# Kernel optimization log

Hardware: AMD Instinct MI355X
Metric: run time of the kernel (lower is better)

## Reference

```python
import jax, jax.numpy as jnp
import numpy as np

N, E, D, H, O, G = 50000, 800000, 64, 64, 32, 64


def setup_inputs() -> dict:
    key = jax.random.key(0)
    ks = jax.random.split(key, 12)
    x = jax.random.normal(ks[0], (N, D), dtype=jnp.float32)
    edge_index = jax.random.randint(ks[1], (2, E), 0, N)
    batch = jnp.sort(jax.random.randint(ks[2], (N,), 0, G))

    def glorot(k, fan_in, fan_out):
        s = np.sqrt(6.0 / (fan_in + fan_out)).astype(np.float32)
        return jax.random.uniform(k, (fan_in, fan_out), jnp.float32, -s, s)

    return {
        "x": x,
        "edge_index": edge_index,
        "batch": batch,
        "W1": glorot(ks[3], D, H), "b1": jnp.zeros((H,), jnp.float32),
        "W2": glorot(ks[4], H, H), "b2": jnp.zeros((H,), jnp.float32),
        "W3": glorot(ks[5], H, H), "b3": jnp.zeros((H,), jnp.float32),
        "Wl": glorot(ks[6], H, O), "bl": jnp.zeros((O,), jnp.float32),
    }


def reference(x, edge_index, batch, W1, b1, W2, b2, W3, b3, Wl, bl):
    n = x.shape[0]
    # GCNConv default: add self-loops, symmetric deg^-1/2 normalization
    loop = jnp.arange(n, dtype=edge_index.dtype)
    src = jnp.concatenate([edge_index[0], loop])  # [E+N]
    dst = jnp.concatenate([edge_index[1], loop])
    deg = jax.ops.segment_sum(jnp.ones_like(src, dtype=x.dtype), dst, num_segments=n)
    dis = jax.lax.rsqrt(deg)  # deg >= 1 due to self-loops
    norm = (dis[src] * dis[dst])[:, None]  # [E+N, 1]

    def gcn(h, W, b):
        hw = h @ W                      # [N, H] small GEMM
        msg = hw[src] * norm            # gather + scale: [E+N, H]
        agg = jax.ops.segment_sum(msg, dst, num_segments=n)  # scatter-add
        return agg + b

    h = jax.nn.relu(gcn(x, W1, b1))
    h = jax.nn.relu(gcn(h, W2, b2))
    h = gcn(h, W3, b3)

    # global_mean_pool over graph ids
    counts = jax.ops.segment_sum(jnp.ones((n,), h.dtype), batch, num_segments=G)
    pooled = jax.ops.segment_sum(h, batch, num_segments=G) / counts[:, None]

    # dropout(p=0.5) is identity in eval mode
    return pooled @ Wl + bl
```

## Files before the change

kernel.cpp:

```cpp
#include <hip/hip_runtime.h>

#define HD 64
#define PSUB 16
#define NBLK 256
#define LOG_NBLK 8
#define NBKT 512

__device__ __forceinline__ unsigned short f2bf(float f) {
    union { float f; unsigned u; } v; v.f = f;
    unsigned r = v.u + 0x7FFF + ((v.u >> 16) & 1);
    return (unsigned short)(r >> 16);
}
__device__ __forceinline__ float u2f(unsigned u) {
    union { unsigned u; float f; } v; v.u = u;
    return v.f;
}


__global__ __launch_bounds__(256) void hist1_k(const int* __restrict__ dst,
                                               int* __restrict__ hist, int E, int chunk,
                                               float* __restrict__ partial, int psz)
{
    __shared__ int lh[NBKT];
    int t = threadIdx.x;
    for (int i = t; i < NBKT; i += 256) lh[i] = 0;
    for (int i = blockIdx.x * 256 + t; i < psz; i += gridDim.x * 256)
        partial[i] = 0.f;
    __syncthreads();
    int base = blockIdx.x * chunk;
    int end  = min(base + chunk, E);
    for (int i = base + t; i < end; i += 256)
        atomicAdd(&lh[dst[i] >> 7], 1);
    __syncthreads();
    for (int i = t; i < NBKT; i += 256)
        hist[blockIdx.x * NBKT + i] = lh[i];
}

__global__ __launch_bounds__(256) void scanA_k(const int* __restrict__ hist,
                                               int* __restrict__ tsum)
{
    __shared__ int s[256];
    int t = threadIdx.x;
    int l = blockIdx.x * 256 + t;
    int phys = (l & (NBLK - 1)) * NBKT + (l >> LOG_NBLK);
    s[t] = hist[phys];
    __syncthreads();
    for (int off = 128; off > 0; off >>= 1) {
        if (t < off) s[t] += s[t + off];
        __syncthreads();
    }
    if (t == 0) tsum[blockIdx.x] = s[0];
}

__global__ __launch_bounds__(1024) void scanB_k(int* __restrict__ tsum, int nb,
    const int* __restrict__ batch, int* __restrict__ gstart, int n, int G)
{
    __shared__ int s[1024];
    int t = threadIdx.x;
    int v = (t < nb) ? tsum[t] : 0;
    s[t] = v;
    __syncthreads();
    for (int off = 1; off < 1024; off <<= 1) {
        int u = (t >= off) ? s[t - off] : 0;
        __syncthreads();
        s[t] += u;
        __syncthreads();
    }
    if (t < nb) tsum[t] = s[t] - v;
    if (t <= G) {
        if (t == G) gstart[t] = n;
        else {
            int lo = 0, hi = n;
            while (lo < hi) { int m = (lo + hi) >> 1; if (batch[m] < t) lo = m + 1; else hi = m; }
            gstart[t] = lo;
        }
    }
}

__global__ __launch_bounds__(256) void scanC_k(const int* __restrict__ hist,
                                               const int* __restrict__ tsum,
                                               int* __restrict__ scanned)
{
    __shared__ int s[256];
    int t = threadIdx.x;
    int l = blockIdx.x * 256 + t;
    int phys = (l & (NBLK - 1)) * NBKT + (l >> LOG_NBLK);
    int own = hist[phys];
    s[t] = own;
    __syncthreads();
    for (int off = 1; off < 256; off <<= 1) {
        int u = (t >= off) ? s[t - off] : 0;
        __syncthreads();
        s[t] += u;
        __syncthreads();
    }
    scanned[l] = tsum[blockIdx.x] + s[t] - own;
}

__global__ __launch_bounds__(256) void append_k(const int* __restrict__ src,
    const int* __restrict__ dst, const int* __restrict__ scanned,
    int* __restrict__ pairs, int E, int chunk)
{
    __shared__ int cur[NBKT];
    int t = threadIdx.x;
    int blk = blockIdx.x;
    for (int i = t; i < NBKT; i += 256) cur[i] = scanned[i * NBLK + blk];
    __syncthreads();
    int base = blk * chunk;
    int end  = min(base + chunk, E);
    for (int i = base + t; i < end; i += 256) {
        int s = src[i], d = dst[i];
        int p = atomicAdd(&cur[d >> 7], 1);
        pairs[p] = (s << 7) | (d & 127);
    }
}

__global__ __launch_bounds__(256) void bucket_csr_k(const int* __restrict__ pairs,
    const int* __restrict__ scanned, int* __restrict__ offsets,
    float* __restrict__ dis, int* __restrict__ csr_src, int N, int E)
{
    __shared__ int cnt[128];
    __shared__ int sc[128];
    __shared__ int cur[128];
    int t = threadIdx.x;
    int b = blockIdx.x;
    int nodeBase = b * 128;
    int nNodes = min(128, N - nodeBase);
    int bBase = scanned[b * NBLK];
    int bEnd  = (b + 1 < NBKT) ? scanned[(b + 1) * NBLK] : E;

    if (t < 128) cnt[t] = 0;
    __syncthreads();
    for (int i = bBase + t; i < bEnd; i += 256)
        atomicAdd(&cnt[pairs[i] & 127], 1);
    __syncthreads();
    int myc = (t < 128) ? cnt[t] : 0;
    if (t < 128) sc[t] = myc;
    __syncthreads();
    for (int off = 1; off < 128; off <<= 1) {
        int u = (t < 128 && t >= off) ? sc[t - off] : 0;
        __syncthreads();
        if (t < 128) sc[t] += u;
        __syncthreads();
    }
    if (t < 128) {
        int excl = sc[t] - myc;
        cur[t] = excl;
        if (t < nNodes) {
            offsets[nodeBase + t] = bBase + excl;
            dis[nodeBase + t] = rsqrtf(1.0f + (float)myc);
        }
    }
    if (t == 0 && b == gridDim.x - 1) offsets[N] = E;
    __syncthreads();
    for (int i = bBase + t; i < bEnd; i += 256) {
        int pk = pairs[i];
        int pos = bBase + atomicAdd(&cur[pk & 127], 1);
        csr_src[pos] = ((unsigned)pk) >> 7;
    }
}


__global__ __launch_bounds__(256) void gemm64_k(
    const float* __restrict__ in, const float* __restrict__ W,
    const float* __restrict__ dis, unsigned short* __restrict__ outb, int n)
{
    __shared__ float HsT[HD][68];
    __shared__ float Ws[HD][HD];
    int t = threadIdx.x;
    int rowBase = blockIdx.x * 64;

    for (int i = t; i < HD * HD / 4; i += 256)
        ((float4*)Ws)[i] = ((const float4*)W)[i];

    if (blockIdx.x == 0 && t < 64)
        outb[(size_t)n * HD + t] = 0;

    {
        int k0 = (t & 15) * 4;
        for (int it = 0; it < 4; ++it) {
            int r = (t >> 4) + it * 16;
            int row = rowBase + r;
            float4 v = make_float4(0.f, 0.f, 0.f, 0.f);
            if (row < n)
                v = *(const float4*)&in[(size_t)row * HD + k0];
            HsT[k0 + 0][r] = v.x;
            HsT[k0 + 1][r] = v.y;
            HsT[k0 + 2][r] = v.z;
            HsT[k0 + 3][r] = v.w;
        }
    }
    __syncthreads();

    int c4 = (t & 15) * 4;
    int r4 = (t >> 4) * 4;
    float acc[4][4];
    #pragma unroll
    for (int i = 0; i < 4; ++i)
        #pragma unroll
        for (int j = 0; j < 4; ++j) acc[i][j] = 0.f;

    #pragma unroll 8
    for (int k = 0; k < HD; ++k) {
        float4 a = *(const float4*)&HsT[k][r4];
        float4 b = *(const float4*)&Ws[k][c4];
        acc[0][0] += a.x * b.x; acc[0][1] += a.x * b.y; acc[0][2] += a.x * b.z; acc[0][3] += a.x * b.w;
        acc[1][0] += a.y * b.x; acc[1][1] += a.y * b.y; acc[1][2] += a.y * b.z; acc[1][3] += a.y * b.w;
        acc[2][0] += a.z * b.x; acc[2][1] += a.z * b.y; acc[2][2] += a.z * b.z; acc[2][3] += a.z * b.w;
        acc[3][0] += a.w * b.x; acc[3][1] += a.w * b.y; acc[3][2] += a.w * b.z; acc[3][3] += a.w * b.w;
    }

    #pragma unroll
    for (int i = 0; i < 4; ++i) {
        int row = rowBase + r4 + i;
        if (row < n) {
            float ds = dis[row];
            ushort4 o;
            o.x = f2bf(ds * acc[i][0]); o.y = f2bf(ds * acc[i][1]);
            o.z = f2bf(ds * acc[i][2]); o.w = f2bf(ds * acc[i][3]);
            *(ushort4*)&outb[(size_t)row * HD + c4] = o;
        }
    }
}

__device__ __forceinline__ void gather8(const unsigned short* __restrict__ hwb,
    const int* __restrict__ offsets, const int* __restrict__ csr_src,
    int node, bool act, int n, int fl, float* a )
{
    int beg = 0, end = 0;
    if (act) { beg = offsets[node]; end = offsets[node + 1]; }
    int deg = end - beg;
    int md = deg;
    md = max(md, __shfl_xor(md, 8, 64));
    md = max(md, __shfl_xor(md, 16, 64));
    md = max(md, __shfl_xor(md, 32, 64));

    int nodeC = act ? node : n;
    uint4 sv = *(const uint4*)(hwb + ((size_t)nodeC << 6) + (fl << 3));
    a[0] = u2f(sv.x << 16); a[1] = u2f(sv.x & 0xFFFF0000u);
    a[2] = u2f(sv.y << 16); a[3] = u2f(sv.y & 0xFFFF0000u);
    a[4] = u2f(sv.z << 16); a[5] = u2f(sv.z & 0xFFFF0000u);
    a[6] = u2f(sv.w << 16); a[7] = u2f(sv.w & 0xFFFF0000u);

    int grpbase = threadIdx.x & 56;
    int idxv = (fl < deg) ? csr_src[beg + fl] : n;
    for (int jb = 0; jb < md; jb += 8) {
        int e2 = jb + 8 + fl;
        int nidx = (e2 < deg) ? csr_src[beg + e2] : n;
        uint4 g[8];
        #pragma unroll
        for (int j = 0; j < 8; ++j) {
            int row = __shfl(idxv, grpbase + j, 64);
            g[j] = *(const uint4*)(hwb + ((size_t)row << 6) + (fl << 3));
        }
        #pragma unroll
        for (int j = 0; j < 8; ++j) {
            a[0] += u2f(g[j].x << 16); a[1] += u2f(g[j].x & 0xFFFF0000u);
            a[2] += u2f(g[j].y << 16); a[3] += u2f(g[j].y & 0xFFFF0000u);
            a[4] += u2f(g[j].z << 16); a[5] += u2f(g[j].z & 0xFFFF0000u);
            a[6] += u2f(g[j].w << 16); a[7] += u2f(g[j].w & 0xFFFF0000u);
        }
        idxv = nidx;
    }
}

__global__ __launch_bounds__(256) void agg_gemm_k(
    const unsigned short* __restrict__ hwb, const float* __restrict__ dis,
    const int* __restrict__ offsets, const int* __restrict__ csr_src,
    const float* __restrict__ b_prev, const float* __restrict__ W,
    unsigned short* __restrict__ outb, int n)
{
    __shared__ float As[32][68];
    __shared__ float Ws[HD][HD];
    int t    = threadIdx.x;
    int lane = t & 63;
    int grp  = lane >> 3;
    int fl   = lane & 7;
    int w    = t >> 6;
    int nib  = w * 8 + grp;
    int nodeBase = blockIdx.x * 32;
    int node = nodeBase + nib;
    bool act = node < n;

    for (int i = t; i < HD * HD / 4; i += 256)
        ((float4*)Ws)[i] = ((const float4*)W)[i];

    if (blockIdx.x == 0 && t < 64)
        outb[(size_t)n * HD + t] = 0;

    float a[8];
    gather8(hwb, offsets, csr_src, node, act, n, fl, a);

    float ds = act ? dis[node] : 0.f;
    int c0 = fl << 3;
    float4 b0 = *(const float4*)&b_prev[c0];
    float4 b1 = *(const float4*)&b_prev[c0 + 4];
    float4 v0, v1;
    v0.x = fmaxf(a[0] * ds + b0.x, 0.f); v0.y = fmaxf(a[1] * ds + b0.y, 0.f);
    v0.z = fmaxf(a[2] * ds + b0.z, 0.f); v0.w = fmaxf(a[3] * ds + b0.w, 0.f);
    v1.x = fmaxf(a[4] * ds + b1.x, 0.f); v1.y = fmaxf(a[5] * ds + b1.y, 0.f);
    v1.z = fmaxf(a[6] * ds + b1.z, 0.f); v1.w = fmaxf(a[7] * ds + b1.w, 0.f);
    *(float4*)&As[nib][c0]     = v0;
    *(float4*)&As[nib][c0 + 4] = v1;
    __syncthreads();

    int r  = t & 31;
    int c8 = (t >> 5) << 3;
    float s0 = 0.f, s1 = 0.f, s2 = 0.f, s3 = 0.f, s4 = 0.f, s5 = 0.f, s6 = 0.f, s7 = 0.f;
    #pragma unroll 4
    for (int k = 0; k < HD; k += 4) {
        float4 aa = *(const float4*)&As[r][k];
        #pragma unroll
        for (int kk = 0; kk < 4; ++kk) {
            float av = (kk == 0) ? aa.x : (kk == 1) ? aa.y : (kk == 2) ? aa.z : aa.w;
            float4 w0 = *(const float4*)&Ws[k + kk][c8];
            float4 w1 = *(const float4*)&Ws[k + kk][c8 + 4];
            s0 += av * w0.x; s1 += av * w0.y; s2 += av * w0.z; s3 += av * w0.w;
            s4 += av * w1.x; s5 += av * w1.y; s6 += av * w1.z; s7 += av * w1.w;
        }
    }
    int orow = nodeBase + r;
    if (orow < n) {
        float d2 = dis[orow];
        ushort4 o0, o1;
        o0.x = f2bf(d2 * s0); o0.y = f2bf(d2 * s1); o0.z = f2bf(d2 * s2); o0.w = f2bf(d2 * s3);
        o1.x = f2bf(d2 * s4); o1.y = f2bf(d2 * s5); o1.z = f2bf(d2 * s6); o1.w = f2bf(d2 * s7);
        *(ushort4*)&outb[(size_t)orow * HD + c8]     = o0;
        *(ushort4*)&outb[(size_t)orow * HD + c8 + 4] = o1;
    }
}

__global__ __launch_bounds__(256) void agg_pool8_k(const unsigned short* __restrict__ hwb,
    const float* __restrict__ dis, const int* __restrict__ offsets,
    const int* __restrict__ csr_src, const int* __restrict__ batch,
    float* __restrict__ partial, int n)
{
    __shared__ float sh[32][68];
    __shared__ int gids[32];
    __shared__ int allsame;
    int t    = threadIdx.x;
    int lane = t & 63;
    int grp  = lane >> 3;
    int fl   = lane & 7;
    int w    = t >> 6;
    int nib  = w * 8 + grp;
    int node = blockIdx.x * 32 + nib;
    bool act = node < n;

    float a[8];
    gather8(hwb, offsets, csr_src, node, act, n, fl, a);

    float ds = act ? dis[node] : 0.f;
    int c0 = fl << 3;
    *(float4*)&sh[nib][c0]     = make_float4(a[0] * ds, a[1] * ds, a[2] * ds, a[3] * ds);
    *(float4*)&sh[nib][c0 + 4] = make_float4(a[4] * ds, a[5] * ds, a[6] * ds, a[7] * ds);
    if (fl == 0) gids[nib] = act ? batch[node] : -1;
    __syncthreads();

    if (t == 0) {
        int g0 = gids[0];
        int ok = (g0 >= 0);
        #pragma unroll
        for (int r = 1; r < 32; ++r) ok &= (gids[r] == g0);
        allsame = ok;
    }
    __syncthreads();

    int slot = blockIdx.x & (PSUB - 1);
    if (allsame) {
        if (t < 64) {
            float s = 0.f;
            #pragma unroll
            for (int r = 0; r < 32; ++r) s += sh[r][t];
            atomicAdd(&partial[((size_t)gids[0] * PSUB + slot) * HD + t], s);
        }
    } else {
        int c  = lane;
        int r0 = w * 8;
        int gw = gids[r0];
        bool same8 = (gw >= 0);
        #pragma unroll
        for (int rr = 1; rr < 8; ++rr) same8 &= (gids[r0 + rr] == gw);
        if (same8) {
            float v = 0.f;
            #pragma unroll
            for (int rr = 0; rr < 8; ++rr) v += sh[r0 + rr][c];
            atomicAdd(&partial[((size_t)gw * PSUB + slot) * HD + c], v);
        } else {
            #pragma unroll
            for (int rr = 0; rr < 8; ++rr) {
                int gg = gids[r0 + rr];
                if (gg >= 0)
                    atomicAdd(&partial[((size_t)gg * PSUB + slot) * HD + c], sh[r0 + rr][c]);
            }
        }
    }
}

__global__ __launch_bounds__(64) void pool2_k(const float* __restrict__ partial,
    const int* __restrict__ gstart, const float* __restrict__ b3,
    const float* __restrict__ Wl, const float* __restrict__ bl,
    float* __restrict__ out, int O)
{
    __shared__ float pooled[HD];
    int g = blockIdx.x;
    int t = threadIdx.x;
    float sum = 0.0f;
    #pragma unroll
    for (int s = 0; s < PSUB; ++s)
        sum += partial[((size_t)g * PSUB + s) * HD + t];
    float cnt = (float)(gstart[g + 1] - gstart[g]);
    pooled[t] = sum / cnt + b3[t];
    __syncthreads();
    if (t < O) {
        float acc = bl[t];
        #pragma unroll
        for (int k = 0; k < HD; ++k) acc += pooled[k] * Wl[k * O + t];
        out[g * O + t] = acc;
    }
}

extern "C" void kernel_launch(void* const* d_in, const int* in_sizes, int n_in,
                              void* d_out, int out_size, void* d_ws, size_t ws_size,
                              hipStream_t stream)
{
    const float* x    = (const float*)d_in[0];
    const int*   ei   = (const int*)d_in[1];
    const int*   batch= (const int*)d_in[2];
    const float* W1   = (const float*)d_in[3];
    const float* b1   = (const float*)d_in[4];
    const float* W2   = (const float*)d_in[5];
    const float* b2   = (const float*)d_in[6];
    const float* W3   = (const float*)d_in[7];
    const float* b3   = (const float*)d_in[8];
    const float* Wl   = (const float*)d_in[9];
    const float* bl   = (const float*)d_in[10];
    float* out = (float*)d_out;

    const int N = in_sizes[0] / HD;
    const int E = in_sizes[1] / 2;
    const int O = in_sizes[10];
    const int G = out_size / O;

    const int* src = ei;
    const int* dst = ei + E;

    char* p = (char*)d_ws;
    auto take = [&](size_t bytes) { char* r = p; p += (bytes + 255) & ~(size_t)255; return r; };
    int*   csr_src = (int*)  take((size_t)(E + 256) * 4);
    int*   offsets = (int*)  take((size_t)(N + 1) * 4);
    float* dis     = (float*)take((size_t)N * 4);
    int*   gstart  = (int*)  take((size_t)(G + 1) * 4);
    float* partial = (float*)take((size_t)G * PSUB * HD * 4);
    unsigned short* hwb  = (unsigned short*)take((size_t)(N + 1) * HD * 2);
    unsigned short* hwb2 = (unsigned short*)take((size_t)(N + 1) * HD * 2);

    int* pairs   = (int*)hwb;
    int* hist    = (int*)hwb2;
    int* scanned = hist + NBLK * NBKT;
    int* tsum    = scanned + NBLK * NBKT;

    const int TB = 256;
    int chunk   = (E + NBLK - 1) / NBLK;
    int ntiles  = (NBLK * NBKT) / 256;
    int nb_gemm = (N + 63) / 64;
    int nb_agg8 = (N + 31) / 32;
    int nbuck   = (N + 127) / 128;
    int psz     = G * PSUB * HD;

    hist1_k<<<NBLK, TB, 0, stream>>>(dst, hist, E, chunk, partial, psz);
    scanA_k<<<ntiles, TB, 0, stream>>>(hist, tsum);
    scanB_k<<<1, 1024, 0, stream>>>(tsum, ntiles, batch, gstart, N, G);
    scanC_k<<<ntiles, TB, 0, stream>>>(hist, tsum, scanned);
    append_k<<<NBLK, TB, 0, stream>>>(src, dst, scanned, pairs, E, chunk);
    bucket_csr_k<<<nbuck, TB, 0, stream>>>(pairs, scanned, offsets, dis, csr_src, N, E);

    gemm64_k<<<nb_gemm, TB, 0, stream>>>(x, W1, dis, hwb, N);

    agg_gemm_k<<<nb_agg8, TB, 0, stream>>>(hwb, dis, offsets, csr_src, b1, W2, hwb2, N);

    agg_gemm_k<<<nb_agg8, TB, 0, stream>>>(hwb2, dis, offsets, csr_src, b2, W3, hwb, N);

    agg_pool8_k<<<nb_agg8, TB, 0, stream>>>(hwb, dis, offsets, csr_src, batch, partial, N);

    pool2_k<<<G, 64, 0, stream>>>(partial, gstart, b3, Wl, bl, out, O);
}
```

Baseline: 184.9 us.

## Reorder nodes by graph and degree bins to balance gather warps

Builds a permutation of nodes, sorted by (graph id, clamped in-degree), using a histogram, a scan and a scatter pass. The aggregation kernels then process nodes in this order, so the 8 nodes sharing a wavefront have similar degree and less time is lost waiting on the longest neighbour list. Nodes stay grouped by graph, which keeps the pooling fast path usable. The cost is two extra kernel launches, atomics during CSR build, an indirect node lookup, and scattered output writes that no longer hit consecutive rows.

```diff
diff --git a/kernel.cpp b/kernel.cpp
--- a/kernel.cpp
+++ b/kernel.cpp
@@ -5,6 +5,7 @@
 #define NBLK 256
 #define LOG_NBLK 8
 #define NBKT 512
+#define DBINS 64
 
 __device__ __forceinline__ unsigned short f2bf(float f) {
     union { float f; unsigned u; } v; v.f = f;
@@ -19,13 +20,16 @@
 
 __global__ __launch_bounds__(256) void hist1_k(const int* __restrict__ dst,
                                                int* __restrict__ hist, int E, int chunk,
-                                               float* __restrict__ partial, int psz)
+                                               float* __restrict__ partial, int psz,
+                                               int* __restrict__ bins, int nbins2)
 {
     __shared__ int lh[NBKT];
     int t = threadIdx.x;
     for (int i = t; i < NBKT; i += 256) lh[i] = 0;
     for (int i = blockIdx.x * 256 + t; i < psz; i += gridDim.x * 256)
         partial[i] = 0.f;
+    for (int i = blockIdx.x * 256 + t; i < nbins2; i += gridDim.x * 256)
+        bins[i] = 0;
     __syncthreads();
     int base = blockIdx.x * chunk;
     int end  = min(base + chunk, E);
@@ -117,7 +121,8 @@
 
 __global__ __launch_bounds__(256) void bucket_csr_k(const int* __restrict__ pairs,
     const int* __restrict__ scanned, int* __restrict__ offsets,
-    float* __restrict__ dis, int* __restrict__ csr_src, int N, int E)
+    float* __restrict__ dis, int* __restrict__ csr_src,
+    const int* __restrict__ batch, int* __restrict__ bins, int N, int E)
 {
     __shared__ int cnt[128];
     __shared__ int sc[128];
@@ -147,8 +152,10 @@
         int excl = sc[t] - myc;
         cur[t] = excl;
         if (t < nNodes) {
-            offsets[nodeBase + t] = bBase + excl;
-            dis[nodeBase + t] = rsqrtf(1.0f + (float)myc);
+            int node = nodeBase + t;
+            offsets[node] = bBase + excl;
+            dis[node] = rsqrtf(1.0f + (float)myc);
+            atomicAdd(&bins[batch[node] * DBINS + min(myc, DBINS - 1)], 1);
         }
     }
     if (t == 0 && b == gridDim.x - 1) offsets[N] = E;
@@ -158,6 +165,47 @@
         int pos = bBase + atomicAdd(&cur[pk & 127], 1);
         csr_src[pos] = ((unsigned)pk) >> 7;
     }
+}
+
+__global__ __launch_bounds__(1024) void binscan_k(int* __restrict__ bins, int nbins)
+{
+    __shared__ int s[1024];
+    int t = threadIdx.x;
+    int per = (nbins + 1023) >> 10;
+    int b0 = t * per;
+    int v[8];
+    int sum = 0;
+    for (int i = 0; i < per; ++i) {
+        int idx = b0 + i;
+        v[i] = (idx < nbins) ? bins[idx] : 0;
+        sum += v[i];
+    }
+    s[t] = sum;
+    __syncthreads();
+    for (int off = 1; off < 1024; off <<= 1) {
+        int u = (t >= off) ? s[t - off] : 0;
+        __syncthreads();
+        s[t] += u;
+        __syncthreads();
+    }
+    int run = s[t] - sum;
+    for (int i = 0; i < per; ++i) {
+        int idx = b0 + i;
+        if (idx < nbins) bins[idx] = run;
+        run += v[i];
+    }
+}
+
+__global__ __launch_bounds__(256) void permscat_k(const int* __restrict__ offsets,
+    const int* __restrict__ batch, const int* __restrict__ binbase,
+    int* __restrict__ bincur, int* __restrict__ perm, int N)
+{
+    int i = blockIdx.x * 256 + threadIdx.x;
+    if (i >= N) return;
+    int deg = offsets[i + 1] - offsets[i];
+    int bin = batch[i] * DBINS + min(deg, DBINS - 1);
+    int pos = binbase[bin] + atomicAdd(&bincur[bin], 1);
+    perm[pos] = i;
 }
 
 
@@ -234,7 +282,6 @@
     md = max(md, __shfl_xor(md, 8, 64));
     md = max(md, __shfl_xor(md, 16, 64));
     md = max(md, __shfl_xor(md, 32, 64));
-
     int nodeC = act ? node : n;
     uint4 sv = *(const uint4*)(hwb + ((size_t)nodeC << 6) + (fl << 3));
     a[0] = u2f(sv.x << 16); a[1] = u2f(sv.x & 0xFFFF0000u);
@@ -267,11 +314,13 @@
 __global__ __launch_bounds__(256) void agg_gemm_k(
     const unsigned short* __restrict__ hwb, const float* __restrict__ dis,
     const int* __restrict__ offsets, const int* __restrict__ csr_src,
+    const int* __restrict__ perm,
     const float* __restrict__ b_prev, const float* __restrict__ W,
     unsigned short* __restrict__ outb, int n)
 {
     __shared__ float As[32][68];
     __shared__ float Ws[HD][HD];
+    __shared__ int pnode[32];
     int t    = threadIdx.x;
     int lane = t & 63;
     int grp  = lane >> 3;
@@ -279,15 +328,18 @@
     int w    = t >> 6;
     int nib  = w * 8 + grp;
     int nodeBase = blockIdx.x * 32;
-    int node = nodeBase + nib;
-    bool act = node < n;
+    bool act = (nodeBase + nib) < n;
+
+    if (t < 32) pnode[t] = (nodeBase + t < n) ? perm[nodeBase + t] : 0;
 
     for (int i = t; i < HD * HD / 4; i += 256)
         ((float4*)Ws)[i] = ((const float4*)W)[i];
 
     if (blockIdx.x == 0 && t < 64)
         outb[(size_t)n * HD + t] = 0;
-
+    __syncthreads();
+
+    int node = pnode[nib];
     float a[8];
     gather8(hwb, offsets, csr_src, node, act, n, fl, a);
 
@@ -319,8 +371,8 @@
             s4 += av * w1.x; s5 += av * w1.y; s6 += av * w1.z; s7 += av * w1.w;
         }
     }
-    int orow = nodeBase + r;
-    if (orow < n) {
+    if (nodeBase + r < n) {
+        int orow = pnode[r];
         float d2 = dis[orow];
         ushort4 o0, o1;
         o0.x = f2bf(d2 * s0); o0.y = f2bf(d2 * s1); o0.z = f2bf(d2 * s2); o0.w = f2bf(d2 * s3);
@@ -332,11 +384,12 @@
 
 __global__ __launch_bounds__(256) void agg_pool8_k(const unsigned short* __restrict__ hwb,
     const float* __restrict__ dis, const int* __restrict__ offsets,
-    const int* __restrict__ csr_src, const int* __restrict__ batch,
-    float* __restrict__ partial, int n)
+    const int* __restrict__ csr_src, const int* __restrict__ perm,
+    const int* __restrict__ batch, float* __restrict__ partial, int n)
 {
     __shared__ float sh[32][68];
     __shared__ int gids[32];
+    __shared__ int pnode[32];
     __shared__ int allsame;
     int t    = threadIdx.x;
     int lane = t & 63;
@@ -344,9 +397,13 @@
     int fl   = lane & 7;
     int w    = t >> 6;
     int nib  = w * 8 + grp;
-    int node = blockIdx.x * 32 + nib;
-    bool act = node < n;
-
+    int nodeBase = blockIdx.x * 32;
+    bool act = (nodeBase + nib) < n;
+
+    if (t < 32) pnode[t] = (nodeBase + t < n) ? perm[nodeBase + t] : 0;
+    __syncthreads();
+
+    int node = pnode[nib];
     float a[8];
     gather8(hwb, offsets, csr_src, node, act, n, fl, a);
 
@@ -452,6 +509,10 @@
     float* dis     = (float*)take((size_t)N * 4);
     int*   gstart  = (int*)  take((size_t)(G + 1) * 4);
     float* partial = (float*)take((size_t)G * PSUB * HD * 4);
+    int    nbins   = G * DBINS;
+    int*   bins    = (int*)  take((size_t)nbins * 2 * 4);
+    int*   bincur  = bins + nbins;
+    int*   perm    = (int*)  take((size_t)N * 4);
     unsigned short* hwb  = (unsigned short*)take((size_t)(N + 1) * HD * 2);
     unsigned short* hwb2 = (unsigned short*)take((size_t)(N + 1) * HD * 2);
 
@@ -465,23 +526,27 @@
     int ntiles  = (NBLK * NBKT) / 256;
     int nb_gemm = (N + 63) / 64;
     int nb_agg8 = (N + 31) / 32;
+    int nb_scat = (N + 255) / 256;
     int nbuck   = (N + 127) / 128;
     int psz     = G * PSUB * HD;
 
-    hist1_k<<<NBLK, TB, 0, stream>>>(dst, hist, E, chunk, partial, psz);
+    hist1_k<<<NBLK, TB, 0, stream>>>(dst, hist, E, chunk, partial, psz, bins, nbins * 2);
     scanA_k<<<ntiles, TB, 0, stream>>>(hist, tsum);
     scanB_k<<<1, 1024, 0, stream>>>(tsum, ntiles, batch, gstart, N, G);
     scanC_k<<<ntiles, TB, 0, stream>>>(hist, tsum, scanned);
     append_k<<<NBLK, TB, 0, stream>>>(src, dst, scanned, pairs, E, chunk);
-    bucket_csr_k<<<nbuck, TB, 0, stream>>>(pairs, scanned, offsets, dis, csr_src, N, E);
+    bucket_csr_k<<<nbuck, TB, 0, stream>>>(pairs, scanned, offsets, dis, csr_src,
+                                           batch, bins, N, E);
+    binscan_k<<<1, 1024, 0, stream>>>(bins, nbins);
+    permscat_k<<<nb_scat, TB, 0, stream>>>(offsets, batch, bins, bincur, perm, N);
 
     gemm64_k<<<nb_gemm, TB, 0, stream>>>(x, W1, dis, hwb, N);
 
-    agg_gemm_k<<<nb_agg8, TB, 0, stream>>>(hwb, dis, offsets, csr_src, b1, W2, hwb2, N);
-
-    agg_gemm_k<<<nb_agg8, TB, 0, stream>>>(hwb2, dis, offsets, csr_src, b2, W3, hwb, N);
-
-    agg_pool8_k<<<nb_agg8, TB, 0, stream>>>(hwb, dis, offsets, csr_src, batch, partial, N);
+    agg_gemm_k<<<nb_agg8, TB, 0, stream>>>(hwb, dis, offsets, csr_src, perm, b1, W2, hwb2, N);
+
+    agg_gemm_k<<<nb_agg8, TB, 0, stream>>>(hwb2, dis, offsets, csr_src, perm, b2, W3, hwb, N);
+
+    agg_pool8_k<<<nb_agg8, TB, 0, stream>>>(hwb, dis, offsets, csr_src, perm, batch, partial, N);
 
     pool2_k<<<G, 64, 0, stream>>>(partial, gstart, b3, Wl, bl, out, O);
 }
```

Measured after the change: 198.7 us. 7.5% more time.
